# Performance work log

Hardware: AMD Instinct MI355X
Metric: run time of the kernel (lower is better)

## Reference

```python
import jax, jax.numpy as jnp
import numpy as np

EPS = 1e-5

def layer_norm(x, gamma, beta):
    mu = jnp.mean(x, axis=-1, keepdims=True)
    var = jnp.mean(jnp.square(x - mu), axis=-1, keepdims=True)
    return (x - mu) * jax.lax.rsqrt(var + EPS) * gamma + beta

def setup_inputs() -> dict:
    key = jax.random.key(0)
    ks = jax.random.split(key, 12)
    B, N, F, H, K = 32, 2048, 128, 256, 64
    A_hat = jax.random.uniform(ks[0], (B, N, N), dtype=jnp.float32) / N  # row-normalized-ish adjacency
    X = jax.random.normal(ks[1], (B, N, F), dtype=jnp.float32)
    def lin(k, din, dout):
        s = 1.0 / np.sqrt(din)
        k1, k2 = jax.random.split(k)
        W = jax.random.uniform(k1, (din, dout), minval=-s, maxval=s, dtype=jnp.float32)
        b = jax.random.uniform(k2, (dout,), minval=-s, maxval=s, dtype=jnp.float32)
        return W, b
    W1, b1 = lin(ks[2], F, H)
    W2, b2 = lin(ks[3], H, H)
    Wa, ba = lin(ks[4], H, K)
    Wl, bl = lin(ks[5], H, K)
    g1 = jnp.ones((H,), jnp.float32); beta1 = jnp.zeros((H,), jnp.float32)
    g2 = jnp.ones((H,), jnp.float32); beta2 = jnp.zeros((H,), jnp.float32)
    return {"A_hat": A_hat, "X": X, "W1": W1, "b1": b1, "g1": g1, "beta1": beta1,
            "W2": W2, "b2": b2, "g2": g2, "beta2": beta2,
            "Wa": Wa, "ba": ba, "Wl": Wl, "bl": bl}

def reference(A_hat, X, W1, b1, g1, beta1, W2, b2, g2, beta2, Wa, ba, Wl, bl):
    # Layer 1: aggregate -> linear -> LayerNorm -> ReLU (dropout is eval identity)
    H = jnp.einsum('bnm,bmf->bnf', A_hat, X)
    H = jnp.einsum('bnf,fh->bnh', H, W1) + b1
    H = jax.nn.relu(layer_norm(H, g1, beta1))
    # Layer 2
    H = jnp.einsum('bnm,bmh->bnh', A_hat, H)
    H = jnp.einsum('bnh,hk->bnk', H, W2) + b2
    H = jax.nn.relu(layer_norm(H, g2, beta2))
    # mean readout over nodes
    g = jnp.mean(H, axis=1)
    pred_arr_reg = g @ Wa + ba
    logits = g @ Wl + bl
    return (pred_arr_reg, logits)
```

## Files before the change

kernel.cpp:

```cpp
#include <hip/hip_runtime.h>
#include <hip/hip_bf16.h>

#define NN 2048

typedef __attribute__((ext_vector_type(4))) float f32x4;
typedef __attribute__((ext_vector_type(8))) short bf16x8;

__device__ __forceinline__ unsigned short f2bf(float f) {
  __hip_bfloat16 h = __float2bfloat16(f);
  return __builtin_bit_cast(unsigned short, h);
}
__device__ __forceinline__ unsigned int pk2(float a, float b) {
  return (unsigned int)f2bf(a) | ((unsigned int)f2bf(b) << 16);
}
__device__ __forceinline__ void gld_lds16(const void* g, void* l) {
  __builtin_amdgcn_global_load_lds(
      (const __attribute__((address_space(1))) unsigned int*)g,
      (__attribute__((address_space(3))) unsigned int*)l, 16, 0, 0);
}

__global__ void k_tr_cvt(const float* __restrict__ src, unsigned short* __restrict__ dst,
                         int R, int C) {
  int b = blockIdx.z;
  src += (size_t)b * R * C;
  dst += (size_t)b * R * C;
  __shared__ float tile[32][33];
  int r0 = blockIdx.x * 32, c0 = blockIdx.y * 32;
  int t = threadIdx.x;
  int r = t >> 3, c4 = (t & 7) << 2;
  float4 v = *(const float4*)(src + (size_t)(r0 + r) * C + c0 + c4);
  tile[r][c4 + 0] = v.x; tile[r][c4 + 1] = v.y; tile[r][c4 + 2] = v.z; tile[r][c4 + 3] = v.w;
  __syncthreads();
  ushort4 o;
  o.x = f2bf(tile[c4 + 0][r]); o.y = f2bf(tile[c4 + 1][r]);
  o.z = f2bf(tile[c4 + 2][r]); o.w = f2bf(tile[c4 + 3][r]);
  *(ushort4*)(dst + (size_t)(c0 + r) * R + r0 + c4) = o;
}

#define AGG_STEP(KT, AREGC, AREGN, CUR)                                        \
  {                                                                            \
    const int kt_ = (KT);                                                      \
    if (kt_ < NKT - 2) {                           \
      const float* p_ = apb + (size_t)(kt_ + 2) * 64;                          \
      _Pragma("unroll") for (int j = 0; j < 4; ++j)                            \
          AREGN[j] = ((const float4*)p_)[j];                                   \
    }                                                                          \
    if (kt_ < NKT - 1) {                                                       \
      _Pragma("unroll") for (int i = 0; i < NF; ++i) {        \
        int jj = i * 512 + t;                                                  \
        int n_ = jj >> 3, s_ = jj & 7, sp_ = s_ ^ (n_ & 7);                    \
        gld_lds16(BTb + (size_t)n_ * NN + (size_t)(kt_ + 1) * 64 + sp_ * 8,    \
                  &Bs[(CUR) ^ 1][(i * 512 + wid * 64) * 8]);                   \
      }                                                                        \
      _Pragma("unroll") for (int i = 0; i < 2; ++i) {     \
        uint4 w_;                                                              \
        w_.x = pk2(AREGC[2 * i].x, AREGC[2 * i].y);                            \
        w_.y = pk2(AREGC[2 * i].z, AREGC[2 * i].w);                            \
        w_.z = pk2(AREGC[2 * i + 1].x, AREGC[2 * i + 1].y);                    \
        w_.w = pk2(AREGC[2 * i + 1].z, AREGC[2 * i + 1].w);                    \
        int s_ = ak * 2 + i, sp_ = s_ ^ (ar & 7);                              \
        *(uint4*)&As[(CUR) ^ 1][(ar * 8 + sp_) * 8] = w_;                      \
      }                                                                        \
    }                                                                          \
    _Pragma("unroll") for (int kh = 0; kh < 2; ++kh) {                         \
      bf16x8 af[4], bfr[NF];                                                   \
      _Pragma("unroll") for (int mi = 0; mi < 4; ++mi) {                       \
        int row = wr * 64 + mi * 16 + lr;                                      \
        int sp_ = (kh * 4 + q) ^ (row & 7);                                    \
        af[mi] = *(const bf16x8*)&As[CUR][(row * 8 + sp_) * 8];                \
      }                                                                        \
      _Pragma("unroll") for (int ni = 0; ni < NF; ++ni) {                      \
        int brow = wc * WN + ni * 16 + lr;                                     \
        int sp_ = (kh * 4 + q) ^ (brow & 7);                                   \
        bfr[ni] = *(const bf16x8*)&Bs[CUR][(brow * 8 + sp_) * 8];              \
      }                                                                        \
      _Pragma("unroll") for (int mi = 0; mi < 4; ++mi)                         \
        _Pragma("unroll") for (int ni = 0; ni < NF; ++ni)                      \
          acc[mi][ni] = __builtin_amdgcn_mfma_f32_16x16x32_bf16(               \
              af[mi], bfr[ni], acc[mi][ni], 0, 0, 0);                          \
    }                                                                          \
    __syncthreads();                                                           \
  }

template <int NCOLS, int MODE>
__global__ __launch_bounds__(512, NCOLS == 128 ? 4 : 2) void k_agg_fused(
    const float* __restrict__ A, const unsigned short* __restrict__ BT,
    const unsigned short* __restrict__ WT, const float* __restrict__ bias,
    const float* __restrict__ gamma, const float* __restrict__ beta,
    unsigned short* __restrict__ HTout, float* __restrict__ gpart) {
  constexpr int WN = NCOLS / 4;
  constexpr int NF = NCOLS / 64;
  constexpr int NKT = NN / 64;
  constexpr int FIN = NCOLS;
  constexpr int NQT = FIN / 64;

  __shared__ __align__(16) unsigned short As[2][128 * 64];
  __shared__ __align__(16) unsigned short Bs[2][NCOLS * 64];
  __shared__ float red[2][128][4];

  int b = blockIdx.z;
  const float* Ab = A + (size_t)b * NN * NN;
  const unsigned short* BTb = BT + (size_t)b * (size_t)NCOLS * NN;
  int m0 = blockIdx.x * 128;
  int t = threadIdx.x, lane = t & 63, wid = t >> 6;
  int wr = wid >> 2, wc = wid & 3;
  int q = lane >> 4, lr = lane & 15;
  int ar = t >> 2, ak = t & 3;
  const float* apb = Ab + (size_t)(m0 + ar) * NN + ak * 16;

  f32x4 acc[4][NF] = {};
  float4 aregA[4], aregB[4];

  {
#pragma unroll
    for (int j = 0; j < 4; ++j) aregA[j] = ((const float4*)apb)[j];
#pragma unroll
    for (int i = 0; i < NF; ++i) {
      int jj = i * 512 + t;
      int n = jj >> 3, s = jj & 7, sp = s ^ (n & 7);
      gld_lds16(BTb + (size_t)n * NN + sp * 8, &Bs[0][(i * 512 + wid * 64) * 8]);
    }
#pragma unroll
    for (int i = 0; i < 2; ++i) {
      uint4 w;
      w.x = pk2(aregA[2 * i].x, aregA[2 * i].y);
      w.y = pk2(aregA[2 * i].z, aregA[2 * i].w);
      w.z = pk2(aregA[2 * i + 1].x, aregA[2 * i + 1].y);
      w.w = pk2(aregA[2 * i + 1].z, aregA[2 * i + 1].w);
      int s = ak * 2 + i, sp = s ^ (ar & 7);
      *(uint4*)&As[0][(ar * 8 + sp) * 8] = w;
    }
#pragma unroll
    for (int j = 0; j < 4; ++j) aregB[j] = ((const float4*)(apb + 64))[j];
  }
  __syncthreads();

  for (int k2 = 0; k2 < NKT / 2; ++k2) {
    AGG_STEP(2 * k2, aregB, aregA, 0);
    AGG_STEP(2 * k2 + 1, aregA, aregB, 1);
  }

  unsigned short* Hs = (NCOLS == 128) ? &As[0][0] : &Bs[0][0];
  unsigned short* Ws = (NCOLS == 128) ? &Bs[0][0] : &As[0][0];
#pragma unroll
  for (int mi = 0; mi < 4; ++mi) {
#pragma unroll
    for (int ni = 0; ni < NF; ++ni) {
#pragma unroll
      for (int j = 0; j < 4; ++j) {
        int row = wr * 64 + mi * 16 + q * 4 + j;
        int col = wc * WN + ni * 16 + lr;
        int sp = (col >> 3) ^ (row & 7);
        Hs[row * FIN + sp * 8 + (col & 7)] = f2bf(acc[mi][ni][j]);
      }
    }
  }

  f32x4 acc2[4][4] = {};
  for (int qt = 0; qt < NQT; ++qt) {
    __syncthreads();
#pragma unroll
    for (int i = 0; i < 4; ++i) {
      int jj = i * 512 + t;
      int h = jj >> 3, s = jj & 7, sp = s ^ (h & 7);
      gld_lds16(WT + (size_t)h * FIN + qt * 64 + sp * 8, Ws + (i * 512 + wid * 64) * 8);
    }
    __syncthreads();
#pragma unroll
    for (int kh = 0; kh < 2; ++kh) {
      bf16x8 hf[4], wf[4];
#pragma unroll
      for (int mi = 0; mi < 4; ++mi) {
        int row = wr * 64 + mi * 16 + lr;
        int slot = qt * 8 + kh * 4 + q;
        int sp = slot ^ (row & 7);
        hf[mi] = *(const bf16x8*)&Hs[row * FIN + sp * 8];
      }
#pragma unroll
      for (int ni = 0; ni < 4; ++ni) {
        int h = wc * 64 + ni * 16 + lr;
        int sp = (kh * 4 + q) ^ (h & 7);
        wf[ni] = *(const bf16x8*)&Ws[(h * 8 + sp) * 8];
      }
#pragma unroll
      for (int mi = 0; mi < 4; ++mi) {
#pragma unroll
        for (int ni = 0; ni < 4; ++ni)
          acc2[mi][ni] = __builtin_amdgcn_mfma_f32_16x16x32_bf16(hf[mi], wf[ni], acc2[mi][ni], 0, 0, 0);
      }
    }
  }

  float bcol[4], gcol[4], zcol[4];
#pragma unroll
  for (int ni = 0; ni < 4; ++ni) {
    int col = wc * 64 + ni * 16 + lr;
    bcol[ni] = bias[col]; gcol[ni] = gamma[col]; zcol[ni] = beta[col];
  }
#pragma unroll
  for (int mi = 0; mi < 4; ++mi) {
#pragma unroll
    for (int j = 0; j < 4; ++j) {
      float s = 0.f, ss = 0.f;
#pragma unroll
      for (int ni = 0; ni < 4; ++ni) {
        float v = acc2[mi][ni][j] + bcol[ni];
        acc2[mi][ni][j] = v;
        s += v; ss += v * v;
      }
#pragma unroll
      for (int m = 1; m < 16; m <<= 1) { s += __shfl_xor(s, m); ss += __shfl_xor(ss, m); }
      if (lr == 0) {
        int rl = wr * 64 + mi * 16 + q * 4 + j;
        red[0][rl][wc] = s;
        red[1][rl][wc] = ss;
      }
    }
  }
  __syncthreads();
#pragma unroll
  for (int mi = 0; mi < 4; ++mi) {
#pragma unroll
    for (int j = 0; j < 4; ++j) {
      int rl = wr * 64 + mi * 16 + q * 4 + j;
      float s = red[0][rl][0] + red[0][rl][1] + red[0][rl][2] + red[0][rl][3];
      float ss = red[1][rl][0] + red[1][rl][1] + red[1][rl][2] + red[1][rl][3];
      float mean = s * (1.f / 256.f);
      float var = ss * (1.f / 256.f) - mean * mean;
      float inv = rsqrtf(var + 1e-5f);
#pragma unroll
      for (int ni = 0; ni < 4; ++ni) {
        float v = (acc2[mi][ni][j] - mean) * inv * gcol[ni] + zcol[ni];
        acc2[mi][ni][j] = v > 0.f ? v : 0.f;
      }
    }
  }
  if (MODE == 0) {
#pragma unroll
    for (int mi = 0; mi < 4; ++mi) {
#pragma unroll
      for (int ni = 0; ni < 4; ++ni) {
        int col = wc * 64 + ni * 16 + lr;
        int rowb = m0 + wr * 64 + mi * 16 + q * 4;
        ushort4 o;
        o.x = f2bf(acc2[mi][ni][0]); o.y = f2bf(acc2[mi][ni][1]);
        o.z = f2bf(acc2[mi][ni][2]); o.w = f2bf(acc2[mi][ni][3]);
        *(ushort4*)(HTout + ((size_t)b * 256 + col) * NN + rowb) = o;
      }
    }
  } else {
#pragma unroll
    for (int ni = 0; ni < 4; ++ni) {
      float cs = 0.f;
#pragma unroll
      for (int mi = 0; mi < 4; ++mi) {
#pragma unroll
        for (int j = 0; j < 4; ++j) cs += acc2[mi][ni][j];
      }
      cs += __shfl_xor(cs, 16);
      cs += __shfl_xor(cs, 32);
      if (q == 0) {
        int col = wc * 64 + ni * 16 + lr;
        gpart[(((size_t)b * 16 + blockIdx.x) * 2 + wr) * 256 + col] = cs;
      }
    }
  }
}

__global__ void k_readout(const float* __restrict__ gpart, const float* __restrict__ Wa,
                          const float* __restrict__ ba, const float* __restrict__ Wl,
                          const float* __restrict__ bl, float* __restrict__ out) {
  __shared__ float gl[256];
  int b = blockIdx.x, t = threadIdx.x;
  float s = 0.f;
#pragma unroll 4
  for (int p = 0; p < 32; ++p) s += gpart[((size_t)b * 32 + p) * 256 + t];
  gl[t] = s * (1.f / 2048.f);
  __syncthreads();
  if (t < 128) {
    int k = t & 63;
    const float* W = (t >= 64) ? Wl : Wa;
    const float* bb = (t >= 64) ? bl : ba;
    float a = 0.f;
    for (int h = 0; h < 256; ++h) a += gl[h] * W[h * 64 + k];
    a += bb[k];
    out[((t >= 64) ? 2048 : 0) + b * 64 + k] = a;
  }
}

extern "C" void kernel_launch(void* const* d_in, const int* in_sizes, int n_in,
                              void* d_out, int out_size, void* d_ws, size_t ws_size,
                              hipStream_t stream) {
  const float* A_hat = (const float*)d_in[0];
  const float* X   = (const float*)d_in[1];
  const float* W1  = (const float*)d_in[2];
  const float* b1  = (const float*)d_in[3];
  const float* g1  = (const float*)d_in[4];
  const float* be1 = (const float*)d_in[5];
  const float* W2  = (const float*)d_in[6];
  const float* b2  = (const float*)d_in[7];
  const float* g2  = (const float*)d_in[8];
  const float* be2 = (const float*)d_in[9];
  const float* Wa  = (const float*)d_in[10];
  const float* ba  = (const float*)d_in[11];
  const float* Wl  = (const float*)d_in[12];
  const float* bl  = (const float*)d_in[13];

  char* ws = (char*)d_ws;
  const size_t MB = 1024 * 1024;
  unsigned short* XT  = (unsigned short*)(ws);
  unsigned short* H1T = (unsigned short*)(ws + 16 * MB);
  unsigned short* W1T = (unsigned short*)(ws + 48 * MB);
  unsigned short* W2T = (unsigned short*)(ws + 48 * MB + 256 * 1024);
  float* gpart        = (float*)(ws + 49 * MB);

  k_tr_cvt<<<dim3(64, 4, 32), 256, 0, stream>>>(X, XT, 2048, 128);
  k_tr_cvt<<<dim3(4, 8, 1), 256, 0, stream>>>(W1, W1T, 128, 256);
  k_tr_cvt<<<dim3(8, 8, 1), 256, 0, stream>>>(W2, W2T, 256, 256);
  k_agg_fused<128, 0><<<dim3(16, 1, 32), 512, 0, stream>>>(
      A_hat, XT, W1T, b1, g1, be1, H1T, nullptr);
  k_agg_fused<256, 1><<<dim3(16, 1, 32), 512, 0, stream>>>(
      A_hat, H1T, W2T, b2, g2, be2, nullptr, gpart);
  k_readout<<<dim3(32), 256, 0, stream>>>(gpart, Wa, ba, Wl, bl, (float*)d_out);
}
```

Measured before the change: 338.0 us.

## Halve layer-2 row tile, remap blocks per XCD, use nontemporal A loads

Templates the fused aggregation kernel on the row-tile size and uses 64-row tiles for the second layer (256 columns), doubling its grid so more blocks fit per CU and the launch bound rises to 4 waves. Blocks are remapped so that each XCD works on the same batch's adjacency and B matrix, which should improve L2 reuse. A loads become nontemporal, and shared memory is merged into one buffer that is aliased for the reduction scratch. The cost is more redundant B-tile loads per output row and an added barrier, and the readout now sums 64 partials per graph.

```diff
diff --git a/kernel.cpp b/kernel.cpp
--- a/kernel.cpp
+++ b/kernel.cpp
@@ -17,6 +17,9 @@
   __builtin_amdgcn_global_load_lds(
       (const __attribute__((address_space(1))) unsigned int*)g,
       (__attribute__((address_space(3))) unsigned int*)l, 16, 0, 0);
+}
+__device__ __forceinline__ f32x4 ntl(const float* p) {
+  return __builtin_nontemporal_load((const f32x4*)p);
 }
 
 __global__ void k_tr_cvt(const float* __restrict__ src, unsigned short* __restrict__ dst,
@@ -37,44 +40,48 @@
   *(ushort4*)(dst + (size_t)(c0 + r) * R + r0 + c4) = o;
 }
 
+#define ASP(bf) (As0 + (bf) * (BM * 64))
+#define BSP(bf) (Bs0 + (bf) * (NCOLS * 64))
+#define RED(sx, rl, w) redp[(((sx) * BM) + (rl)) * 4 + (w)]
+
 #define AGG_STEP(KT, AREGC, AREGN, CUR)                                        \
   {                                                                            \
     const int kt_ = (KT);                                                      \
-    if (kt_ < NKT - 2) {                           \
+    if (kt_ < NKT - 2) {                                                       \
       const float* p_ = apb + (size_t)(kt_ + 2) * 64;                          \
-      _Pragma("unroll") for (int j = 0; j < 4; ++j)                            \
-          AREGN[j] = ((const float4*)p_)[j];                                   \
+      _Pragma("unroll") for (int j = 0; j < F4; ++j)                           \
+          AREGN[j] = ntl(p_ + j * 4);                                          \
     }                                                                          \
     if (kt_ < NKT - 1) {                                                       \
-      _Pragma("unroll") for (int i = 0; i < NF; ++i) {        \
+      _Pragma("unroll") for (int i = 0; i < NF; ++i) {                         \
         int jj = i * 512 + t;                                                  \
         int n_ = jj >> 3, s_ = jj & 7, sp_ = s_ ^ (n_ & 7);                    \
         gld_lds16(BTb + (size_t)n_ * NN + (size_t)(kt_ + 1) * 64 + sp_ * 8,    \
-                  &Bs[(CUR) ^ 1][(i * 512 + wid * 64) * 8]);                   \
+                  BSP((CUR) ^ 1) + (i * 512 + wid * 64) * 8);                  \
       }                                                                        \
-      _Pragma("unroll") for (int i = 0; i < 2; ++i) {     \
+      _Pragma("unroll") for (int i = 0; i < U4W; ++i) {                        \
         uint4 w_;                                                              \
-        w_.x = pk2(AREGC[2 * i].x, AREGC[2 * i].y);                            \
-        w_.y = pk2(AREGC[2 * i].z, AREGC[2 * i].w);                            \
-        w_.z = pk2(AREGC[2 * i + 1].x, AREGC[2 * i + 1].y);                    \
-        w_.w = pk2(AREGC[2 * i + 1].z, AREGC[2 * i + 1].w);                    \
-        int s_ = ak * 2 + i, sp_ = s_ ^ (ar & 7);                              \
-        *(uint4*)&As[(CUR) ^ 1][(ar * 8 + sp_) * 8] = w_;                      \
+        w_.x = pk2(AREGC[2 * i][0], AREGC[2 * i][1]);                          \
+        w_.y = pk2(AREGC[2 * i][2], AREGC[2 * i][3]);                          \
+        w_.z = pk2(AREGC[2 * i + 1][0], AREGC[2 * i + 1][1]);                  \
+        w_.w = pk2(AREGC[2 * i + 1][2], AREGC[2 * i + 1][3]);                  \
+        int s_ = ak * U4W + i, sp_ = s_ ^ (ar & 7);                            \
+        *(uint4*)(ASP((CUR) ^ 1) + (ar * 8 + sp_) * 8) = w_;                   \
       }                                                                        \
     }                                                                          \
     _Pragma("unroll") for (int kh = 0; kh < 2; ++kh) {                         \
-      bf16x8 af[4], bfr[NF];                                                   \
-      _Pragma("unroll") for (int mi = 0; mi < 4; ++mi) {                       \
-        int row = wr * 64 + mi * 16 + lr;                                      \
+      bf16x8 af[MI], bfr[NF];                                                  \
+      _Pragma("unroll") for (int mi = 0; mi < MI; ++mi) {                      \
+        int row = wr * (BM / 2) + mi * 16 + lr;                                \
         int sp_ = (kh * 4 + q) ^ (row & 7);                                    \
-        af[mi] = *(const bf16x8*)&As[CUR][(row * 8 + sp_) * 8];                \
+        af[mi] = *(const bf16x8*)(ASP(CUR) + (row * 8 + sp_) * 8);             \
       }                                                                        \
       _Pragma("unroll") for (int ni = 0; ni < NF; ++ni) {                      \
         int brow = wc * WN + ni * 16 + lr;                                     \
         int sp_ = (kh * 4 + q) ^ (brow & 7);                                   \
-        bfr[ni] = *(const bf16x8*)&Bs[CUR][(brow * 8 + sp_) * 8];              \
+        bfr[ni] = *(const bf16x8*)(BSP(CUR) + (brow * 8 + sp_) * 8);           \
       }                                                                        \
-      _Pragma("unroll") for (int mi = 0; mi < 4; ++mi)                         \
+      _Pragma("unroll") for (int mi = 0; mi < MI; ++mi)                        \
         _Pragma("unroll") for (int ni = 0; ni < NF; ++ni)                      \
           acc[mi][ni] = __builtin_amdgcn_mfma_f32_16x16x32_bf16(               \
               af[mi], bfr[ni], acc[mi][ni], 0, 0, 0);                          \
@@ -82,56 +89,69 @@
     __syncthreads();                                                           \
   }
 
-template <int NCOLS, int MODE>
-__global__ __launch_bounds__(512, NCOLS == 128 ? 4 : 2) void k_agg_fused(
+template <int BM, int NCOLS, int MODE>
+__global__ __launch_bounds__(512, 4) void k_agg_fused(
     const float* __restrict__ A, const unsigned short* __restrict__ BT,
     const unsigned short* __restrict__ WT, const float* __restrict__ bias,
     const float* __restrict__ gamma, const float* __restrict__ beta,
     unsigned short* __restrict__ HTout, float* __restrict__ gpart) {
   constexpr int WN = NCOLS / 4;
   constexpr int NF = NCOLS / 64;
+  constexpr int MI = BM / 32;
   constexpr int NKT = NN / 64;
   constexpr int FIN = NCOLS;
   constexpr int NQT = FIN / 64;
-
-  __shared__ __align__(16) unsigned short As[2][128 * 64];
-  __shared__ __align__(16) unsigned short Bs[2][NCOLS * 64];
-  __shared__ float red[2][128][4];
-
-  int b = blockIdx.z;
+  constexpr int TPR = 512 / BM;
+  constexpr int FPT = BM * 64 / 512;
+  constexpr int F4 = FPT / 4;
+  constexpr int U4W = F4 / 2;
+  constexpr int NMB = NN / BM;
+  constexpr int AS_B = 2 * BM * 64 * 2;
+  constexpr int BS_B = 2 * NCOLS * 64 * 2;
+
+  __shared__ __align__(16) char smem[AS_B + BS_B];
+  unsigned short* As0 = (unsigned short*)smem;
+  unsigned short* Bs0 = (unsigned short*)(smem + AS_B);
+  float* redp = (float*)smem;
+
+  int L = blockIdx.x + gridDim.x * blockIdx.z;
+  int xcd = L & 7, slot = L >> 3;
+  int mb = slot % NMB;
+  int b = xcd + 8 * (slot / NMB);
+  int m0 = mb * BM;
+
   const float* Ab = A + (size_t)b * NN * NN;
   const unsigned short* BTb = BT + (size_t)b * (size_t)NCOLS * NN;
-  int m0 = blockIdx.x * 128;
   int t = threadIdx.x, lane = t & 63, wid = t >> 6;
   int wr = wid >> 2, wc = wid & 3;
   int q = lane >> 4, lr = lane & 15;
-  int ar = t >> 2, ak = t & 3;
-  const float* apb = Ab + (size_t)(m0 + ar) * NN + ak * 16;
-
-  f32x4 acc[4][NF] = {};
-  float4 aregA[4], aregB[4];
+  int ar = t / TPR, ak = t % TPR;
+  const float* apb = Ab + (size_t)(m0 + ar) * NN + ak * FPT;
+
+  f32x4 acc[MI][NF] = {};
+  f32x4 aregA[F4], aregB[F4];
 
   {
 #pragma unroll
-    for (int j = 0; j < 4; ++j) aregA[j] = ((const float4*)apb)[j];
+    for (int j = 0; j < F4; ++j) aregA[j] = ntl(apb + j * 4);
 #pragma unroll
     for (int i = 0; i < NF; ++i) {
       int jj = i * 512 + t;
       int n = jj >> 3, s = jj & 7, sp = s ^ (n & 7);
-      gld_lds16(BTb + (size_t)n * NN + sp * 8, &Bs[0][(i * 512 + wid * 64) * 8]);
-    }
-#pragma unroll
-    for (int i = 0; i < 2; ++i) {
+      gld_lds16(BTb + (size_t)n * NN + sp * 8, BSP(0) + (i * 512 + wid * 64) * 8);
+    }
+#pragma unroll
+    for (int i = 0; i < U4W; ++i) {
       uint4 w;
-      w.x = pk2(aregA[2 * i].x, aregA[2 * i].y);
-      w.y = pk2(aregA[2 * i].z, aregA[2 * i].w);
-      w.z = pk2(aregA[2 * i + 1].x, aregA[2 * i + 1].y);
-      w.w = pk2(aregA[2 * i + 1].z, aregA[2 * i + 1].w);
-      int s = ak * 2 + i, sp = s ^ (ar & 7);
-      *(uint4*)&As[0][(ar * 8 + sp) * 8] = w;
-    }
-#pragma unroll
-    for (int j = 0; j < 4; ++j) aregB[j] = ((const float4*)(apb + 64))[j];
+      w.x = pk2(aregA[2 * i][0], aregA[2 * i][1]);
+      w.y = pk2(aregA[2 * i][2], aregA[2 * i][3]);
+      w.z = pk2(aregA[2 * i + 1][0], aregA[2 * i + 1][1]);
+      w.w = pk2(aregA[2 * i + 1][2], aregA[2 * i + 1][3]);
+      int s = ak * U4W + i, sp = s ^ (ar & 7);
+      *(uint4*)(ASP(0) + (ar * 8 + sp) * 8) = w;
+    }
+#pragma unroll
+    for (int j = 0; j < F4; ++j) aregB[j] = ntl(apb + 64 + j * 4);
   }
   __syncthreads();
 
@@ -140,15 +160,15 @@
     AGG_STEP(2 * k2 + 1, aregA, aregB, 1);
   }
 
-  unsigned short* Hs = (NCOLS == 128) ? &As[0][0] : &Bs[0][0];
-  unsigned short* Ws = (NCOLS == 128) ? &Bs[0][0] : &As[0][0];
-#pragma unroll
-  for (int mi = 0; mi < 4; ++mi) {
+  unsigned short* Hs = (NCOLS == 128) ? As0 : Bs0;
+  unsigned short* Ws = (NCOLS == 128) ? Bs0 : Bs0 + NCOLS * 64;
+#pragma unroll
+  for (int mi = 0; mi < MI; ++mi) {
 #pragma unroll
     for (int ni = 0; ni < NF; ++ni) {
 #pragma unroll
       for (int j = 0; j < 4; ++j) {
-        int row = wr * 64 + mi * 16 + q * 4 + j;
+        int row = wr * (BM / 2) + mi * 16 + q * 4 + j;
         int col = wc * WN + ni * 16 + lr;
         int sp = (col >> 3) ^ (row & 7);
         Hs[row * FIN + sp * 8 + (col & 7)] = f2bf(acc[mi][ni][j]);
@@ -156,7 +176,7 @@
     }
   }
 
-  f32x4 acc2[4][4] = {};
+  f32x4 acc2[MI][4] = {};
   for (int qt = 0; qt < NQT; ++qt) {
     __syncthreads();
 #pragma unroll
@@ -168,12 +188,12 @@
     __syncthreads();
 #pragma unroll
     for (int kh = 0; kh < 2; ++kh) {
-      bf16x8 hf[4], wf[4];
-#pragma unroll
-      for (int mi = 0; mi < 4; ++mi) {
-        int row = wr * 64 + mi * 16 + lr;
-        int slot = qt * 8 + kh * 4 + q;
-        int sp = slot ^ (row & 7);
+      bf16x8 hf[MI], wf[4];
+#pragma unroll
+      for (int mi = 0; mi < MI; ++mi) {
+        int row = wr * (BM / 2) + mi * 16 + lr;
+        int slotk = qt * 8 + kh * 4 + q;
+        int sp = slotk ^ (row & 7);
         hf[mi] = *(const bf16x8*)&Hs[row * FIN + sp * 8];
       }
 #pragma unroll
@@ -183,13 +203,14 @@
         wf[ni] = *(const bf16x8*)&Ws[(h * 8 + sp) * 8];
       }
 #pragma unroll
-      for (int mi = 0; mi < 4; ++mi) {
+      for (int mi = 0; mi < MI; ++mi) {
 #pragma unroll
         for (int ni = 0; ni < 4; ++ni)
           acc2[mi][ni] = __builtin_amdgcn_mfma_f32_16x16x32_bf16(hf[mi], wf[ni], acc2[mi][ni], 0, 0, 0);
       }
     }
   }
+  __syncthreads();
 
   float bcol[4], gcol[4], zcol[4];
 #pragma unroll
@@ -198,7 +219,7 @@
     bcol[ni] = bias[col]; gcol[ni] = gamma[col]; zcol[ni] = beta[col];
   }
 #pragma unroll
-  for (int mi = 0; mi < 4; ++mi) {
+  for (int mi = 0; mi < MI; ++mi) {
 #pragma unroll
     for (int j = 0; j < 4; ++j) {
       float s = 0.f, ss = 0.f;
@@ -211,20 +232,20 @@
 #pragma unroll
       for (int m = 1; m < 16; m <<= 1) { s += __shfl_xor(s, m); ss += __shfl_xor(ss, m); }
       if (lr == 0) {
-        int rl = wr * 64 + mi * 16 + q * 4 + j;
-        red[0][rl][wc] = s;
-        red[1][rl][wc] = ss;
-      }
-    }
-  }
-  __syncthreads();
-#pragma unroll
-  for (int mi = 0; mi < 4; ++mi) {
+        int rl = wr * (BM / 2) + mi * 16 + q * 4 + j;
+        RED(0, rl, wc) = s;
+        RED(1, rl, wc) = ss;
+      }
+    }
+  }
+  __syncthreads();
+#pragma unroll
+  for (int mi = 0; mi < MI; ++mi) {
 #pragma unroll
     for (int j = 0; j < 4; ++j) {
-      int rl = wr * 64 + mi * 16 + q * 4 + j;
-      float s = red[0][rl][0] + red[0][rl][1] + red[0][rl][2] + red[0][rl][3];
-      float ss = red[1][rl][0] + red[1][rl][1] + red[1][rl][2] + red[1][rl][3];
+      int rl = wr * (BM / 2) + mi * 16 + q * 4 + j;
+      float s = RED(0, rl, 0) + RED(0, rl, 1) + RED(0, rl, 2) + RED(0, rl, 3);
+      float ss = RED(1, rl, 0) + RED(1, rl, 1) + RED(1, rl, 2) + RED(1, rl, 3);
       float mean = s * (1.f / 256.f);
       float var = ss * (1.f / 256.f) - mean * mean;
       float inv = rsqrtf(var + 1e-5f);
@@ -237,11 +258,11 @@
   }
   if (MODE == 0) {
 #pragma unroll
-    for (int mi = 0; mi < 4; ++mi) {
+    for (int mi = 0; mi < MI; ++mi) {
 #pragma unroll
       for (int ni = 0; ni < 4; ++ni) {
         int col = wc * 64 + ni * 16 + lr;
-        int rowb = m0 + wr * 64 + mi * 16 + q * 4;
+        int rowb = m0 + wr * (BM / 2) + mi * 16 + q * 4;
         ushort4 o;
         o.x = f2bf(acc2[mi][ni][0]); o.y = f2bf(acc2[mi][ni][1]);
         o.z = f2bf(acc2[mi][ni][2]); o.w = f2bf(acc2[mi][ni][3]);
@@ -253,7 +274,7 @@
     for (int ni = 0; ni < 4; ++ni) {
       float cs = 0.f;
 #pragma unroll
-      for (int mi = 0; mi < 4; ++mi) {
+      for (int mi = 0; mi < MI; ++mi) {
 #pragma unroll
         for (int j = 0; j < 4; ++j) cs += acc2[mi][ni][j];
       }
@@ -261,7 +282,7 @@
       cs += __shfl_xor(cs, 32);
       if (q == 0) {
         int col = wc * 64 + ni * 16 + lr;
-        gpart[(((size_t)b * 16 + blockIdx.x) * 2 + wr) * 256 + col] = cs;
+        gpart[(((size_t)b * NMB + mb) * 2 + wr) * 256 + col] = cs;
       }
     }
   }
@@ -274,7 +295,7 @@
   int b = blockIdx.x, t = threadIdx.x;
   float s = 0.f;
 #pragma unroll 4
-  for (int p = 0; p < 32; ++p) s += gpart[((size_t)b * 32 + p) * 256 + t];
+  for (int p = 0; p < 64; ++p) s += gpart[((size_t)b * 64 + p) * 256 + t];
   gl[t] = s * (1.f / 2048.f);
   __syncthreads();
   if (t < 128) {
@@ -317,9 +338,9 @@
   k_tr_cvt<<<dim3(64, 4, 32), 256, 0, stream>>>(X, XT, 2048, 128);
   k_tr_cvt<<<dim3(4, 8, 1), 256, 0, stream>>>(W1, W1T, 128, 256);
   k_tr_cvt<<<dim3(8, 8, 1), 256, 0, stream>>>(W2, W2T, 256, 256);
-  k_agg_fused<128, 0><<<dim3(16, 1, 32), 512, 0, stream>>>(
+  k_agg_fused<128, 128, 0><<<dim3(16, 1, 32), 512, 0, stream>>>(
       A_hat, XT, W1T, b1, g1, be1, H1T, nullptr);
-  k_agg_fused<256, 1><<<dim3(16, 1, 32), 512, 0, stream>>>(
+  k_agg_fused<64, 256, 1><<<dim3(32, 1, 32), 512, 0, stream>>>(
       A_hat, H1T, W2T, b2, g2, be2, nullptr, gpart);
   k_readout<<<dim3(32), 256, 0, stream>>>(gpart, Wa, ba, Wl, bl, (float*)d_out);
 }
```

Result: slower. 396.1 us (+17.2%).
